# Optimization experiments

Measured on AMD Instinct MI355X. Metric: run time of the kernel, lower is better.

## Reference

```python
import jax, jax.numpy as jnp
import numpy as np

M, N, K, C, H = 100000, 8192, 32, 256, 8
DH = C // H
FF = 512
R = (15, 15, 7)  # 2*MAXRANGE-1 per axis for MAXRANGE=[8,8,4]


def _layer_norm(x, g, b, eps=1e-5):
    mu = jnp.mean(x, axis=-1, keepdims=True)
    xc = x - mu
    var = jnp.mean(xc * xc, axis=-1, keepdims=True)
    return xc * jax.lax.rsqrt(var + eps) * g + b


def setup_inputs() -> dict:
    key = jax.random.key(0)
    ks = iter(jax.random.split(key, 40))
    d = {}
    d['voxel_features'] = jax.random.normal(next(ks), (M, C), jnp.float32)
    d['query_coords'] = jax.random.normal(next(ks), (N, 3), jnp.float32)
    d['query_indices'] = jax.random.randint(next(ks), (N,), 0, M)
    d['gather_indices'] = jax.random.randint(next(ks), (N, K), 0, M)
    d['gather_mask'] = jax.random.randint(next(ks), (N, K), 0, 2).astype(bool)
    d['rel_x'] = jax.random.randint(next(ks), (N, K), 0, R[0])
    d['rel_y'] = jax.random.randint(next(ks), (N, K), 0, R[1])
    d['rel_z'] = jax.random.randint(next(ks), (N, K), 0, R[2])
    s = 0.02
    # pos_proj: Conv1d(3, C, 1) == linear on coords
    d['w_pos'] = jax.random.normal(next(ks), (3, C), jnp.float32) * s
    d['b_pos'] = jnp.zeros((C,), jnp.float32)
    for nm in ['q', 'k', 'v', 'proj']:
        d['w_' + nm] = jax.random.normal(next(ks), (C, C), jnp.float32) * (C ** -0.5)
        d['b_' + nm] = jnp.zeros((C,), jnp.float32)
    d['ln1_g'] = jnp.ones((C,), jnp.float32); d['ln1_b'] = jnp.zeros((C,), jnp.float32)
    d['ln2_g'] = jnp.ones((C,), jnp.float32); d['ln2_b'] = jnp.zeros((C,), jnp.float32)
    d['w_ff1'] = jax.random.normal(next(ks), (C, FF), jnp.float32) * (C ** -0.5)
    d['b_ff1'] = jnp.zeros((FF,), jnp.float32)
    d['w_ff2'] = jax.random.normal(next(ks), (FF, C), jnp.float32) * (FF ** -0.5)
    d['b_ff2'] = jnp.zeros((C,), jnp.float32)
    # per-axis relative position tables: [H, DH, 2W-1] for q-side and k-side
    for m in ['q', 'k']:
        for ax, r in zip(['x', 'y', 'z'], R):
            d[f'pos_{m}{ax}'] = jax.random.normal(next(ks), (H, DH, r), jnp.float32) * s
    return d


def reference(voxel_features, query_coords, query_indices, gather_indices, gather_mask,
              rel_x, rel_y, rel_z,
              w_pos, b_pos, w_q, b_q, w_k, b_k, w_v, b_v, w_proj, b_proj,
              ln1_g, ln1_b, ln2_g, ln2_b, w_ff1, b_ff1, w_ff2, b_ff2,
              pos_qx, pos_qy, pos_qz, pos_kx, pos_ky, pos_kz):
    x = _layer_norm(voxel_features, ln1_g, ln1_b)           # [M, C] pre-norm
    # gather window centers (queries) + positional projection of coords
    q_in = x[query_indices] + jax.nn.relu(query_coords @ w_pos + b_pos)  # [N, C]
    kv_in = x[gather_indices]                                # [N, K, C]
    kv_in = jnp.where(gather_mask[..., None], 0.0, kv_in)
    q = (q_in @ w_q + b_q).reshape(N, H, DH)
    k = (kv_in @ w_k + b_k).reshape(N, K, H, DH)
    v = (kv_in @ w_v + b_v).reshape(N, K, H, DH)
    logits = jnp.einsum('nhd,nkhd->nhk', q, k) * (DH ** -0.5)  # [N, H, K]
    # query-side per-axis relative position bias: contract q with table, gather at rel idx
    for pos, rel in ((pos_qx, rel_x), (pos_qy, rel_y), (pos_qz, rel_z)):
        qp = jnp.einsum('nhd,hdr->nhr', q, pos)              # [N, H, R]
        logits = logits + jnp.take_along_axis(qp, rel[:, None, :], axis=2)
    # key-side per-axis relative position bias
    for pos, rel in ((pos_kx, rel_x), (pos_ky, rel_y), (pos_kz, rel_z)):
        kp = jnp.einsum('nkhd,hdr->nkhr', k, pos)            # [N, K, H, R]
        bias = jnp.take_along_axis(kp, rel[:, :, None, None], axis=3)[..., 0]  # [N, K, H]
        logits = logits + bias.transpose(0, 2, 1)
    logits = jnp.where(gather_mask[:, None, :], -1e9, logits)
    attn = jax.nn.softmax(logits, axis=-1)
    out = jnp.einsum('nhk,nkhd->nhd', attn, v).reshape(N, C) @ w_proj + b_proj
    act = voxel_features[query_indices] + out                # residual (pre-norm block)
    h = jax.nn.relu(_layer_norm(act, ln2_g, ln2_b) @ w_ff1 + b_ff1) @ w_ff2 + b_ff2
    return act + h                                           # [N, C]
```

## Files before the change

### kernel.cpp

```cpp
#include <hip/hip_runtime.h>
#include <hip/hip_bf16.h>
#include <math.h>

#define MV   100000
#define NQ   8192
#define KN   32
#define CH   256
#define NH   8
#define DHD  32
#define FFD  512
#define NG   (NQ*KN)
#define QPW  37
#define QPN  (NH*QPW)
#define QPL  320
#define ASTR 40
#define KSTR 264

typedef __bf16 bf16x8 __attribute__((ext_vector_type(8)));
typedef float  f32x4  __attribute__((ext_vector_type(4)));

__device__ __forceinline__ float bf2f(unsigned short u) {
    return __uint_as_float(((unsigned int)u) << 16);
}
__device__ __forceinline__ unsigned short f2bf(float f) {
    unsigned int x = __float_as_uint(f);
    unsigned int r = x + 0x7FFFu + ((x >> 16) & 1u);
    return (unsigned short)(r >> 16);
}
__device__ __forceinline__ void glds16(const unsigned short* g, unsigned short* l) {
    __builtin_amdgcn_global_load_lds(
        (const __attribute__((address_space(1))) void*)g,
        (__attribute__((address_space(3))) void*)l, 16, 0, 0);
}

__global__ __launch_bounds__(256) void k_detect_mask(const unsigned char* __restrict__ raw,
                                                     int* __restrict__ flags) {
    __shared__ int any;
    if (threadIdx.x == 0) any = 0;
    __syncthreads();
    const uint4* p = (const uint4*)raw;
    int i = blockIdx.x * 256 + threadIdx.x;
    uint4 v = p[i];
    if ((v.x | v.y | v.z | v.w) & 0xFFFFFF00u) any = 1;
    __syncthreads();
    if (threadIdx.x == 0) flags[blockIdx.x] = any;
}

__global__ __launch_bounds__(256) void k_prep(const float* __restrict__ w_k,
                                              const float* __restrict__ w_v,
                                              const float* __restrict__ w_ff1,
                                              const float* __restrict__ w_ff2,
                                              const float* __restrict__ w_proj,
                                              const float* __restrict__ w_q,
                                              const float* __restrict__ b_k,
                                              const float* __restrict__ b_v,
                                              const float* __restrict__ pos_qx,
                                              const float* __restrict__ pos_qy,
                                              const float* __restrict__ pos_qz,
                                              const void* __restrict__ mask_raw,
                                              const int* __restrict__ gidx,
                                              const int* __restrict__ flags,
                                              unsigned short* __restrict__ w_kv_t,
                                              unsigned short* __restrict__ w1_t,
                                              unsigned short* __restrict__ w2_t,
                                              unsigned short* __restrict__ wp_t,
                                              unsigned short* __restrict__ wq_t,
                                              unsigned short* __restrict__ wqp_t,
                                              float* __restrict__ bkv,
                                              float* __restrict__ zbias,
                                              int* __restrict__ mask_i,
                                              unsigned char* __restrict__ touched) {
    __shared__ int bl;
    if (threadIdx.x == 0) {
        int a = 0;
        #pragma unroll 8
        for (int i = 0; i < 64; i++) a |= flags[i];
        bl = a;
    }
    __syncthreads();
    int byteLayout = bl;
    int idx = blockIdx.x * 256 + threadIdx.x;
    if (blockIdx.x == 0 && threadIdx.x < 512)
        bkv[threadIdx.x] = (threadIdx.x < 256) ? b_k[threadIdx.x]
                                               : b_v[threadIdx.x - 256];
    if (idx < QPL) zbias[idx] = 0.f;
    if (idx < NG) {
        int mv = byteLayout ? (int)((const unsigned char*)mask_raw)[idx]
                            : ((const int*)mask_raw)[idx];
        mask_i[idx] = (mv != 0) ? 1 : 0;
        if (mv == 0) touched[gidx[idx]] = 1;
    }
    if (idx < 512 * 256) {
        int col = idx >> 8, j = idx & 255;
        float v = (col < 256) ? w_k[j * 256 + col] : w_v[j * 256 + (col - 256)];
        w_kv_t[idx] = f2bf(v);
    }
    if (idx < 512 * 256) {
        int n = idx >> 8, k = idx & 255;
        w1_t[idx] = f2bf(w_ff1[k * FFD + n]);
    }
    if (idx < 256 * 512) {
        int n = idx >> 9, k = idx & 511;
        w2_t[idx] = f2bf(w_ff2[k * CH + n]);
    }
    if (idx < 256 * 256) {
        int n = idx >> 8, k = idx & 255;
        wp_t[idx] = f2bf(w_proj[k * CH + n]);
        wq_t[idx] = f2bf(w_q[k * CH + n]);
    }
    if (idx < QPL * 256) {
        int col = idx >> 8, k = idx & 255;
        float v = 0.f;
        if (col < QPN) {
            int h = col / QPW, r = col % QPW;
            int h2 = k >> 5, d = k & 31;
            if (h2 == h) {
                if (r < 15)      v = pos_qx[(h * DHD + d) * 15 + r];
                else if (r < 30) v = pos_qy[(h * DHD + d) * 15 + (r - 15)];
                else             v = pos_qz[(h * DHD + d) * 7  + (r - 30)];
            }
        }
        wqp_t[idx] = f2bf(v);
    }
}

__global__ __launch_bounds__(256) void k_posc(const float* __restrict__ pos_kx,
                                              const float* __restrict__ pos_ky,
                                              const float* __restrict__ pos_kz,
                                              float* __restrict__ comb) {
    int idx = blockIdx.x * 256 + threadIdx.x;
    if (idx >= 8 * 15 * 15 * 7 * 32) return;
    int d = idx & 31, r = idx >> 5;
    int rz = r % 7;  r /= 7;
    int ry = r % 15; r /= 15;
    int rx = r % 15; int h = r / 15;
    comb[idx] = pos_kx[(h * DHD + d) * 15 + rx]
              + pos_ky[(h * DHD + d) * 15 + ry]
              + pos_kz[(h * DHD + d) * 7  + rz];
}

__global__ __launch_bounds__(256) void k_ln(const float* __restrict__ x,
                                            const float* __restrict__ g,
                                            const float* __restrict__ b,
                                            unsigned short* __restrict__ o,
                                            int nrows) {
    int wid = threadIdx.x >> 6, lane = threadIdx.x & 63;
    int row = blockIdx.x * 4 + wid;
    if (row >= nrows) return;
    const float4 v = *(const float4*)(x + (size_t)row * CH + lane * 4);
    float s  = v.x + v.y + v.z + v.w;
    float sq = v.x * v.x + v.y * v.y + v.z * v.z + v.w * v.w;
    #pragma unroll
    for (int off = 1; off < 64; off <<= 1) {
        s  += __shfl_xor(s,  off);
        sq += __shfl_xor(sq, off);
    }
    float mu  = s * (1.f / CH);
    float var = sq * (1.f / CH) - mu * mu;
    float rs  = rsqrtf(var + 1e-5f);
    float4 gv = *(const float4*)(g + lane * 4);
    float4 bv = *(const float4*)(b + lane * 4);
    ushort4 ov;
    ov.x = f2bf((v.x - mu) * rs * gv.x + bv.x);
    ov.y = f2bf((v.y - mu) * rs * gv.y + bv.y);
    ov.z = f2bf((v.z - mu) * rs * gv.z + bv.z);
    ov.w = f2bf((v.w - mu) * rs * gv.w + bv.w);
    *(ushort4*)(o + (size_t)row * CH + lane * 4) = ov;
}

__global__ __launch_bounds__(256) void k_qin(const unsigned short* __restrict__ ln_x,
                                             const float* __restrict__ coords,
                                             const int* __restrict__ qidx,
                                             const float* __restrict__ w_pos,
                                             const float* __restrict__ b_pos,
                                             unsigned short* __restrict__ qin) {
    int c = threadIdx.x;
    int nb = blockIdx.x * 8;
    float wp0 = w_pos[c], wp1 = w_pos[CH + c], wp2 = w_pos[2 * CH + c], bp = b_pos[c];
    #pragma unroll
    for (int qq = 0; qq < 8; qq++) {
        int n = nb + qq;
        float p = bp + coords[n * 3] * wp0 + coords[n * 3 + 1] * wp1 + coords[n * 3 + 2] * wp2;
        p = fmaxf(p, 0.f);
        int qi = qidx[n];
        qin[(size_t)n * CH + c] = f2bf(bf2f(ln_x[(size_t)qi * CH + c]) + p);
    }
}

__global__ __launch_bounds__(256) void k_kv(const unsigned short* __restrict__ ln_x,
                                            const unsigned short* __restrict__ w_kv_t,
                                            const float* __restrict__ bkv,
                                            const unsigned char* __restrict__ touched,
                                            unsigned short* __restrict__ kv) {
    __shared__ __align__(16) unsigned short As[8 * 4096];
    __shared__ __align__(16) unsigned short Bs[4096];
    const int tid = threadIdx.x;
    const int w = tid >> 6, l = tid & 63;
    const int wr = w >> 1, wc = w & 1;
    const int rowbase = blockIdx.x * 128;
    const int sr = l >> 2, sq = l & 3;
    const int ml = l & 15, qd = l >> 4;

    int ra0 = rowbase + w * 16 + sr;
    int ra1 = rowbase + 64 + w * 16 + sr;
    int ok0 = (ra0 < MV) && touched[ra0 < MV ? ra0 : 0];
    int ok1 = (ra1 < MV) && touched[ra1 < MV ? ra1 : 0];
    const unsigned short* pa0 = ln_x + (size_t)(ok0 ? ra0 : rowbase) * CH + sq * 8;
    const unsigned short* pa1 = ln_x + (size_t)(ok1 ? ra1 : rowbase) * CH + sq * 8;
    unsigned short* lA0 = As + w * 512;
    unsigned short* lA1 = As + 2048 + w * 512;
    unsigned short* lB0 = Bs + w * 512;
    unsigned short* lB1 = Bs + 2048 + w * 512;

    #pragma unroll
    for (int c = 0; c < 8; c++) {
        glds16(pa0 + c * 32, lA0 + c * 4096);
        glds16(pa1 + c * 32, lA1 + c * 4096);
    }

    for (int ct = 0; ct < 4; ct++) {
        const int col0 = ct * 128;
        const unsigned short* pb0 = w_kv_t + (size_t)(col0 + w * 16 + sr) * CH + sq * 8;
        const unsigned short* pb1 = w_kv_t + (size_t)(col0 + 64 + w * 16 + sr) * CH + sq * 8;
        f32x4 acc[4][4];
        #pragma unroll
        for (int mt = 0; mt < 4; mt++)
            #pragma unroll
            for (int nt = 0; nt < 4; nt++)
                acc[mt][nt] = (f32x4){0.f, 0.f, 0.f, 0.f};

        for (int c = 0; c < 8; c++) {
            __syncthreads();
            glds16(pb0 + c * 32, lB0);
            glds16(pb1 + c * 32, lB1);
            __syncthreads();
            bf16x8 af[4], bf[4];
            const unsigned short* Ac = As + c * 4096;
            #pragma unroll
            for (int mt = 0; mt < 4; mt++)
                af[mt] = *(const bf16x8*)(Ac + (wr * 64 + mt * 16 + ml) * 32 + qd * 8);
            #pragma unroll
            for (int nt = 0; nt < 4; nt++)
                bf[nt] = *(const bf16x8*)(Bs + (wc * 64 + nt * 16 + ml) * 32 + qd * 8);
            #pragma unroll
            for (int mt = 0; mt < 4; mt++)
                #pragma unroll
                for (int nt = 0; nt < 4; nt++)
                    acc[mt][nt] = __builtin_amdgcn_mfma_f32_16x16x32_bf16(af[mt], bf[nt], acc[mt][nt], 0, 0, 0);
        }

        float bb[4];
        #pragma unroll
        for (int nt = 0; nt < 4; nt++)
            bb[nt] = bkv[col0 + wc * 64 + nt * 16 + ml];
        #pragma unroll
        for (int mt = 0; mt < 4; mt++) {
            __syncthreads();
            #pragma unroll
            for (int nt = 0; nt < 4; nt++) {
                int lcol = wc * 64 + nt * 16 + ml;
                #pragma unroll
                for (int i = 0; i < 4; i++)
                    Bs[wr * 2048 + (qd * 4 + i) * 128 + lcol] = f2bf(acc[mt][nt][i] + bb[nt]);
            }
            __syncthreads();
            int rl = tid >> 4, cc = (tid & 15) * 8;
            int g0 = rowbase + mt * 16 + rl;
            int g1 = rowbase + 64 + mt * 16 + rl;
            if (g0 < MV && touched[g0])
                *(uint4*)(kv + (size_t)g0 * 512 + col0 + cc) = *(const uint4*)(Bs + rl * 128 + cc);
            if (g1 < MV && touched[g1])
                *(uint4*)(kv + (size_t)g1 * 512 + col0 + cc) = *(const uint4*)(Bs + 2048 + rl * 128 + cc);
        }
    }
}

template <int KD, int EPI, int LDO>
__global__ __launch_bounds__(256) void k_mm(const unsigned short* __restrict__ A,
                                            const unsigned short* __restrict__ Bt_g,
                                            const float* __restrict__ bias,
                                            const float* __restrict__ res,
                                            const int* __restrict__ qidx,
                                            unsigned short* __restrict__ out_bf,
                                            float* __restrict__ out_f) {
    __shared__ __align__(16) unsigned short As[128 * ASTR];
    __shared__ __align__(16) unsigned short Bs[64 * ASTR];
    int tid = threadIdx.x;
    int w = tid >> 6, l = tid & 63;
    int rowbase = blockIdx.y * 128;
    int col0 = blockIdx.x * 64;
    int r0 = tid >> 2, qt = tid & 3;
    const unsigned short* a0p = A + (size_t)(rowbase + r0) * KD + qt * 8;
    const unsigned short* a1p = A + (size_t)(rowbase + 64 + r0) * KD + qt * 8;

    f32x4 acc[2][4];
    #pragma unroll
    for (int mt = 0; mt < 2; mt++)
        #pragma unroll
        for (int nt = 0; nt < 4; nt++)
            acc[mt][nt] = (f32x4){0.f, 0.f, 0.f, 0.f};

    const int ml = l & 15, qd = l >> 4;
    for (int kk = 0; kk < KD; kk += 32) {
        __syncthreads();
        uint4 v0 = *(const uint4*)(a0p + kk);
        uint4 v1 = *(const uint4*)(a1p + kk);
        *(uint4*)(As + r0 * ASTR + qt * 8)        = v0;
        *(uint4*)(As + (64 + r0) * ASTR + qt * 8) = v1;
        {
            uint4 bv = *(const uint4*)(Bt_g + (size_t)(col0 + r0) * KD + kk + qt * 8);
            *(uint4*)(Bs + r0 * ASTR + qt * 8) = bv;
        }
        __syncthreads();
        bf16x8 a0 = *(const bf16x8*)(As + (w * 32 + ml) * ASTR + qd * 8);
        bf16x8 a1 = *(const bf16x8*)(As + (w * 32 + 16 + ml) * ASTR + qd * 8);
        #pragma unroll
        for (int nt = 0; nt < 4; nt++) {
            bf16x8 bb = *(const bf16x8*)(Bs + (nt * 16 + ml) * ASTR + qd * 8);
            acc[0][nt] = __builtin_amdgcn_mfma_f32_16x16x32_bf16(a0, bb, acc[0][nt], 0, 0, 0);
            acc[1][nt] = __builtin_amdgcn_mfma_f32_16x16x32_bf16(a1, bb, acc[1][nt], 0, 0, 0);
        }
    }

    #pragma unroll
    for (int nt = 0; nt < 4; nt++) {
        int col = col0 + nt * 16 + ml;
        float bv = bias[col];
        #pragma unroll
        for (int mt = 0; mt < 2; mt++) {
            int rl = w * 32 + mt * 16 + qd * 4;
            #pragma unroll
            for (int i = 0; i < 4; i++) {
                int row = rowbase + rl + i;
                float v = acc[mt][nt][i] + bv;
                if (EPI == 0) {
                    out_bf[(size_t)row * LDO + col] = f2bf(fmaxf(v, 0.f));
                } else if (EPI == 1) {
                    out_f[(size_t)row * CH + col] = v + res[(size_t)row * CH + col];
                } else if (EPI == 2) {
                    int qi = qidx[row];
                    out_f[(size_t)row * CH + col] = v + res[(size_t)qi * CH + col];
                } else if (EPI == 3) {
                    out_f[(size_t)row * CH + col] = v;
                    out_bf[(size_t)row * CH + col] = f2bf(v);
                } else {
                    out_f[(size_t)row * LDO + col] = v;
                }
            }
        }
    }
}

__global__ __launch_bounds__(256) void k_attn3(const float* __restrict__ qbuf,
                                               const float* __restrict__ qp,
                                               const unsigned short* __restrict__ kvmat,
                                               const int* __restrict__ gidx,
                                               const int* __restrict__ mask_i,
                                               const int* __restrict__ rel_x,
                                               const int* __restrict__ rel_y,
                                               const int* __restrict__ rel_z,
                                               const float* __restrict__ comb,
                                               const float* __restrict__ b_v,
                                               unsigned short* __restrict__ attnln) {
    __shared__ float q_s[2 * 256];
    __shared__ float qp_s[2 * QPL];
    __shared__ float attn_s[2 * 256];
    __shared__ int   mask_s[64];
    __shared__ int   gidx_s[64];
    __shared__ __align__(16) unsigned short ks[64 * KSTR];

    int tid = threadIdx.x;
    int qb = blockIdx.x * 2;
    for (int i = tid; i < 512; i += 256) q_s[i] = qbuf[(size_t)qb * CH + i];
    for (int i = tid; i < 2 * QPL; i += 256) qp_s[i] = qp[(size_t)qb * QPL + i];
    if (tid < 64) {
        mask_s[tid] = mask_i[qb * 32 + tid];
        gidx_s[tid] = gidx[qb * 32 + tid];
    }
    __syncthreads();

    const int srow = tid >> 5;
    const int schk = tid & 31;
    uint4 kreg[8];
    #pragma unroll
    for (int j = 0; j < 8; j++) {
        int r = j * 8 + srow;
        uint4 v = {0u, 0u, 0u, 0u};
        if (!mask_s[r])
            v = *(const uint4*)(kvmat + (size_t)gidx_s[r] * 512 + schk * 8);
        kreg[j] = v;
    }
    #pragma unroll
    for (int j = 0; j < 8; j++)
        *(uint4*)(ks + (j * 8 + srow) * KSTR + schk * 8) = kreg[j];
    __syncthreads();

    int h = tid >> 5, k = tid & 31;
    const float scale = 0.17677669529663687f;
    for (int qq = 0; qq < 2; qq++) {
        int n = qb + qq;
        int gi = n * KN + k;
        int r = qq * 32 + k;
        int mk = mask_s[r];
        float lg = -1e9f;
        if (!mk) {
            int rx = rel_x[gi], ry = rel_y[gi], rz = rel_z[gi];
            const unsigned short* kp = ks + r * KSTR + h * 32;
            float kv[32];
            #pragma unroll
            for (int j = 0; j < 4; j++) {
                uint4 u = *(const uint4*)(kp + j * 8);
                kv[j * 8 + 0] = bf2f((unsigned short)(u.x & 0xFFFF));
                kv[j * 8 + 1] = bf2f((unsigned short)(u.x >> 16));
                kv[j * 8 + 2] = bf2f((unsigned short)(u.y & 0xFFFF));
                kv[j * 8 + 3] = bf2f((unsigned short)(u.y >> 16));
                kv[j * 8 + 4] = bf2f((unsigned short)(u.z & 0xFFFF));
                kv[j * 8 + 5] = bf2f((unsigned short)(u.z >> 16));
                kv[j * 8 + 6] = bf2f((unsigned short)(u.w & 0xFFFF));
                kv[j * 8 + 7] = bf2f((unsigned short)(u.w >> 16));
            }
            const float* cp = comb + ((((h * 15 + rx) * 15 + ry) * 7 + rz) << 5);
            float s1 = 0.f, s2 = 0.f;
            const float* qrow = q_s + qq * CH + h * DHD;
            #pragma unroll
            for (int d = 0; d < 32; d++) {
                s1 += kv[d] * qrow[d];
                s2 += kv[d] * cp[d];
            }
            lg = s1 * scale + s2
               + qp_s[qq * QPL + h * QPW + rx]
               + qp_s[qq * QPL + h * QPW + 15 + ry]
               + qp_s[qq * QPL + h * QPW + 30 + rz];
        }
        float mx = lg;
        #pragma unroll
        for (int off = 1; off <= 16; off <<= 1) mx = fmaxf(mx, __shfl_xor(mx, off));
        float e = mk ? 0.f : __expf(lg - mx);
        float sm = e;
        #pragma unroll
        for (int off = 1; off <= 16; off <<= 1) sm += __shfl_xor(sm, off);
        attn_s[qq * 256 + tid] = (sm > 0.f) ? e / sm : 0.f;
    }

    #pragma unroll
    for (int j = 0; j < 8; j++) {
        int r = j * 8 + srow;
        uint4 v = {0u, 0u, 0u, 0u};
        if (!mask_s[r])
            v = *(const uint4*)(kvmat + (size_t)gidx_s[r] * 512 + 256 + schk * 8);
        kreg[j] = v;
    }
    __syncthreads();
    #pragma unroll
    for (int j = 0; j < 8; j++)
        *(uint4*)(ks + (j * 8 + srow) * KSTR + schk * 8) = kreg[j];
    __syncthreads();

    int w = tid >> 6, l = tid & 63;
    int q2 = w >> 1, kh = w & 1;
    int hh = l >> 3;
    float a0 = 0.f, a1 = 0.f, a2 = 0.f, a3 = 0.f;
    #pragma unroll
    for (int i = 0; i < 16; i++) {
        int kk = kh * 16 + i;
        int r = q2 * 32 + kk;
        float av = attn_s[q2 * 256 + hh * 32 + kk];
        ushort4 v4 = *(const ushort4*)(ks + r * KSTR + l * 4);
        a0 += av * bf2f(v4.x);
        a1 += av * bf2f(v4.y);
        a2 += av * bf2f(v4.z);
        a3 += av * bf2f(v4.w);
    }
    if (kh == 1) {
        float4 pv = {a0, a1, a2, a3};
        *(float4*)(qp_s + q2 * 256 + l * 4) = pv;
    }
    __syncthreads();
    if (kh == 0) {
        float4 pv = *(const float4*)(qp_s + q2 * 256 + l * 4);
        a0 += pv.x; a1 += pv.y; a2 += pv.z; a3 += pv.w;
        int nm = 0;
        #pragma unroll
        for (int kk = 0; kk < 32; kk++) nm += 1 - mask_s[q2 * 32 + kk];
        int col = l * 4;
        if (nm == 0) {
            a0 = b_v[col]; a1 = b_v[col + 1]; a2 = b_v[col + 2]; a3 = b_v[col + 3];
        }
        ushort4 o;
        o.x = f2bf(a0); o.y = f2bf(a1); o.z = f2bf(a2); o.w = f2bf(a3);
        *(ushort4*)(attnln + (size_t)(qb + q2) * CH + col) = o;
    }
}

extern "C" void kernel_launch(void* const* d_in, const int* in_sizes, int n_in,
                              void* d_out, int out_size, void* d_ws, size_t ws_size,
                              hipStream_t stream) {
    (void)in_sizes; (void)n_in; (void)out_size; (void)ws_size;
    const float* vox    = (const float*)d_in[0];
    const float* coords = (const float*)d_in[1];
    const int*   qidx   = (const int*)d_in[2];
    const int*   gidx   = (const int*)d_in[3];
    const void*  mraw   = d_in[4];
    const int*   rel_x  = (const int*)d_in[5];
    const int*   rel_y  = (const int*)d_in[6];
    const int*   rel_z  = (const int*)d_in[7];
    const float* w_pos  = (const float*)d_in[8];
    const float* b_pos  = (const float*)d_in[9];
    const float* w_q    = (const float*)d_in[10];
    const float* b_q    = (const float*)d_in[11];
    const float* w_k    = (const float*)d_in[12];
    const float* b_k    = (const float*)d_in[13];
    const float* w_v    = (const float*)d_in[14];
    const float* b_v    = (const float*)d_in[15];
    const float* w_proj = (const float*)d_in[16];
    const float* b_proj = (const float*)d_in[17];
    const float* ln1_g  = (const float*)d_in[18];
    const float* ln1_b  = (const float*)d_in[19];
    const float* ln2_g  = (const float*)d_in[20];
    const float* ln2_b  = (const float*)d_in[21];
    const float* w_ff1  = (const float*)d_in[22];
    const float* b_ff1  = (const float*)d_in[23];
    const float* w_ff2  = (const float*)d_in[24];
    const float* b_ff2  = (const float*)d_in[25];
    const float* pos_qx = (const float*)d_in[26];
    const float* pos_qy = (const float*)d_in[27];
    const float* pos_qz = (const float*)d_in[28];
    const float* pos_kx = (const float*)d_in[29];
    const float* pos_ky = (const float*)d_in[30];
    const float* pos_kz = (const float*)d_in[31];

    char* p = (char*)d_ws;
    auto take = [&](size_t n) { char* r = p; p += (n + 255) & ~(size_t)255; return r; };
    unsigned short* ln_x    = (unsigned short*)take((size_t)MV * CH * 2);
    unsigned short* w_kv_t  = (unsigned short*)take((size_t)512 * 256 * 2);
    unsigned short* w1_t    = (unsigned short*)take((size_t)512 * 256 * 2);
    unsigned short* w2_t    = (unsigned short*)take((size_t)256 * 512 * 2);
    unsigned short* wp_t    = (unsigned short*)take((size_t)256 * 256 * 2);
    unsigned short* wq_t    = (unsigned short*)take((size_t)256 * 256 * 2);
    unsigned short* wqp_t   = (unsigned short*)take((size_t)QPL * 256 * 2);
    float*          bkv     = (float*)take(512 * 4);
    float*          zbias   = (float*)take(QPL * 4);
    int*            flags   = (int*)take(64 * 4);
    int*            mask_i  = (int*)take((size_t)NG * 4);
    unsigned char*  touched = (unsigned char*)take(MV);
    float*          comb    = (float*)take((size_t)8 * 15 * 15 * 7 * 32 * 4);
    unsigned short* qin     = (unsigned short*)take((size_t)NQ * CH * 2);
    float*          qbuf    = (float*)take((size_t)NQ * CH * 4);
    unsigned short* qbf     = (unsigned short*)take((size_t)NQ * CH * 2);
    float*          qp      = (float*)take((size_t)NQ * QPL * 4);
    unsigned short* kvmat   = (unsigned short*)take((size_t)MV * 512 * 2);
    unsigned short* attnln  = (unsigned short*)take((size_t)NQ * CH * 2);
    float*          actbuf  = (float*)take((size_t)NQ * CH * 4);
    unsigned short* actln   = (unsigned short*)take((size_t)NQ * CH * 2);
    unsigned short* hbuf    = (unsigned short*)take((size_t)NQ * FFD * 2);

    hipMemsetAsync(touched, 0, MV, stream);
    hipLaunchKernelGGL(k_detect_mask, dim3(64), dim3(256), 0, stream,
                       (const unsigned char*)mraw, flags);
    hipLaunchKernelGGL(k_prep, dim3(NG / 256), dim3(256), 0, stream,
                       w_k, w_v, w_ff1, w_ff2, w_proj, w_q, b_k, b_v,
                       pos_qx, pos_qy, pos_qz, mraw, gidx, flags,
                       w_kv_t, w1_t, w2_t, wp_t, wq_t, wqp_t, bkv, zbias,
                       mask_i, touched);
    hipLaunchKernelGGL(k_posc, dim3((8 * 15 * 15 * 7 * 32 + 255) / 256), dim3(256), 0, stream,
                       pos_kx, pos_ky, pos_kz, comb);
    hipLaunchKernelGGL(k_ln, dim3(MV / 4 + 1), dim3(256), 0, stream,
                       vox, ln1_g, ln1_b, ln_x, MV);
    hipLaunchKernelGGL(k_qin, dim3(NQ / 8), dim3(256), 0, stream,
                       ln_x, coords, qidx, w_pos, b_pos, qin);
    hipLaunchKernelGGL(k_kv, dim3((MV + 127) / 128), dim3(256), 0, stream,
                       ln_x, w_kv_t, bkv, touched, kvmat);
    hipLaunchKernelGGL(HIP_KERNEL_NAME(k_mm<256, 3, CH>), dim3(4, NQ / 128), dim3(256), 0, stream,
                       qin, wq_t, b_q, (const float*)nullptr, (const int*)nullptr,
                       qbf, qbuf);
    hipLaunchKernelGGL(HIP_KERNEL_NAME(k_mm<256, 4, QPL>), dim3(QPL / 64, NQ / 128), dim3(256), 0, stream,
                       qbf, wqp_t, zbias, (const float*)nullptr, (const int*)nullptr,
                       (unsigned short*)nullptr, qp);
    hipLaunchKernelGGL(k_attn3, dim3(NQ / 2), dim3(256), 0, stream,
                       qbuf, qp, kvmat, gidx, mask_i, rel_x, rel_y, rel_z,
                       comb, b_v, attnln);
    hipLaunchKernelGGL(HIP_KERNEL_NAME(k_mm<256, 2, CH>), dim3(4, NQ / 128), dim3(256), 0, stream,
                       attnln, wp_t, b_proj, vox, qidx,
                       (unsigned short*)nullptr, actbuf);
    hipLaunchKernelGGL(k_ln, dim3(NQ / 4), dim3(256), 0, stream,
                       actbuf, ln2_g, ln2_b, actln, NQ);
    hipLaunchKernelGGL(HIP_KERNEL_NAME(k_mm<256, 0, FFD>), dim3(8, NQ / 128), dim3(256), 0, stream,
                       actln, w1_t, b_ff1, (const float*)nullptr, (const int*)nullptr,
                       hbuf, (float*)nullptr);
    hipLaunchKernelGGL(HIP_KERNEL_NAME(k_mm<512, 1, CH>), dim3(4, NQ / 128), dim3(256), 0, stream,
                       hbuf, w2_t, b_ff2, actbuf, (const int*)nullptr,
                       (unsigned short*)nullptr, (float*)d_out);
}
```

Baseline: 401.8 us.

## Skip LayerNorm on unreferenced voxels and split KV GEMM columns across blocks

Marks query-index rows as touched in the prep kernel, so the first LayerNorm can skip voxel rows that no gather or query ever reads. This saves fp32 reads and bf16 writes on those rows. The KV projection kernel now uses a 2D grid with one 128-column tile per block instead of looping over four column tiles. Its shared memory drops from about 72KB to 16KB, which should allow more resident blocks, at the cost of reloading the A rows four times.

```diff
diff --git a/kernel.cpp b/kernel.cpp
--- a/kernel.cpp
+++ b/kernel.cpp
@@ -59,6 +59,7 @@
                                               const float* __restrict__ pos_qz,
                                               const void* __restrict__ mask_raw,
                                               const int* __restrict__ gidx,
+                                              const int* __restrict__ qidx,
                                               const int* __restrict__ flags,
                                               unsigned short* __restrict__ w_kv_t,
                                               unsigned short* __restrict__ w1_t,
@@ -84,6 +85,7 @@
         bkv[threadIdx.x] = (threadIdx.x < 256) ? b_k[threadIdx.x]
                                                : b_v[threadIdx.x - 256];
     if (idx < QPL) zbias[idx] = 0.f;
+    if (idx < NQ) touched[qidx[idx]] = 1;
     if (idx < NG) {
         int mv = byteLayout ? (int)((const unsigned char*)mask_raw)[idx]
                             : ((const int*)mask_raw)[idx];
@@ -142,11 +144,13 @@
 __global__ __launch_bounds__(256) void k_ln(const float* __restrict__ x,
                                             const float* __restrict__ g,
                                             const float* __restrict__ b,
+                                            const unsigned char* __restrict__ tch,
                                             unsigned short* __restrict__ o,
                                             int nrows) {
     int wid = threadIdx.x >> 6, lane = threadIdx.x & 63;
     int row = blockIdx.x * 4 + wid;
     if (row >= nrows) return;
+    if (tch && !tch[row]) return;
     const float4 v = *(const float4*)(x + (size_t)row * CH + lane * 4);
     float s  = v.x + v.y + v.z + v.w;
     float sq = v.x * v.x + v.y * v.y + v.z * v.z + v.w * v.w;
@@ -192,86 +196,79 @@
                                             const float* __restrict__ bkv,
                                             const unsigned char* __restrict__ touched,
                                             unsigned short* __restrict__ kv) {
-    __shared__ __align__(16) unsigned short As[8 * 4096];
-    __shared__ __align__(16) unsigned short Bs[4096];
+    __shared__ __align__(16) unsigned short As[128 * 32];
+    __shared__ __align__(16) unsigned short Bs[128 * 32];
     const int tid = threadIdx.x;
     const int w = tid >> 6, l = tid & 63;
     const int wr = w >> 1, wc = w & 1;
-    const int rowbase = blockIdx.x * 128;
+    const int rowbase = blockIdx.y * 128;
+    const int col0 = blockIdx.x * 128;
     const int sr = l >> 2, sq = l & 3;
-    const int ml = l & 15, qd = l >> 4;
-
     int ra0 = rowbase + w * 16 + sr;
     int ra1 = rowbase + 64 + w * 16 + sr;
     int ok0 = (ra0 < MV) && touched[ra0 < MV ? ra0 : 0];
     int ok1 = (ra1 < MV) && touched[ra1 < MV ? ra1 : 0];
-    const unsigned short* pa0 = ln_x + (size_t)(ok0 ? ra0 : rowbase) * CH + sq * 8;
-    const unsigned short* pa1 = ln_x + (size_t)(ok1 ? ra1 : rowbase) * CH + sq * 8;
+    const unsigned short* pa0 = ln_x + (size_t)(ok0 ? ra0 : 0) * CH + sq * 8;
+    const unsigned short* pa1 = ln_x + (size_t)(ok1 ? ra1 : 0) * CH + sq * 8;
+    const unsigned short* pb0 = w_kv_t + (size_t)(col0 + w * 16 + sr) * CH + sq * 8;
+    const unsigned short* pb1 = w_kv_t + (size_t)(col0 + 64 + w * 16 + sr) * CH + sq * 8;
     unsigned short* lA0 = As + w * 512;
     unsigned short* lA1 = As + 2048 + w * 512;
     unsigned short* lB0 = Bs + w * 512;
     unsigned short* lB1 = Bs + 2048 + w * 512;
 
-    #pragma unroll
-    for (int c = 0; c < 8; c++) {
-        glds16(pa0 + c * 32, lA0 + c * 4096);
-        glds16(pa1 + c * 32, lA1 + c * 4096);
-    }
-
-    for (int ct = 0; ct < 4; ct++) {
-        const int col0 = ct * 128;
-        const unsigned short* pb0 = w_kv_t + (size_t)(col0 + w * 16 + sr) * CH + sq * 8;
-        const unsigned short* pb1 = w_kv_t + (size_t)(col0 + 64 + w * 16 + sr) * CH + sq * 8;
-        f32x4 acc[4][4];
+    f32x4 acc[4][4];
+    #pragma unroll
+    for (int mt = 0; mt < 4; mt++)
+        #pragma unroll
+        for (int nt = 0; nt < 4; nt++)
+            acc[mt][nt] = (f32x4){0.f, 0.f, 0.f, 0.f};
+
+    const int ml = l & 15, qd = l >> 4;
+    for (int kk = 0; kk < CH; kk += 32) {
+        __syncthreads();
+        glds16(pa0 + kk, lA0);
+        glds16(pa1 + kk, lA1);
+        glds16(pb0 + kk, lB0);
+        glds16(pb1 + kk, lB1);
+        __syncthreads();
+        bf16x8 af[4], bf[4];
+        #pragma unroll
+        for (int mt = 0; mt < 4; mt++)
+            af[mt] = *(const bf16x8*)(As + (wr * 64 + mt * 16 + ml) * 32 + qd * 8);
+        #pragma unroll
+        for (int nt = 0; nt < 4; nt++)
+            bf[nt] = *(const bf16x8*)(Bs + (wc * 64 + nt * 16 + ml) * 32 + qd * 8);
         #pragma unroll
         for (int mt = 0; mt < 4; mt++)
             #pragma unroll
             for (int nt = 0; nt < 4; nt++)
-                acc[mt][nt] = (f32x4){0.f, 0.f, 0.f, 0.f};
-
-        for (int c = 0; c < 8; c++) {
-            __syncthreads();
-            glds16(pb0 + c * 32, lB0);
-            glds16(pb1 + c * 32, lB1);
-            __syncthreads();
-            bf16x8 af[4], bf[4];
-            const unsigned short* Ac = As + c * 4096;
+                acc[mt][nt] = __builtin_amdgcn_mfma_f32_16x16x32_bf16(af[mt], bf[nt], acc[mt][nt], 0, 0, 0);
+    }
+
+    float bb[4];
+    #pragma unroll
+    for (int nt = 0; nt < 4; nt++)
+        bb[nt] = bkv[col0 + wc * 64 + nt * 16 + ml];
+    unsigned short* trs = As;
+    #pragma unroll
+    for (int mt = 0; mt < 4; mt++) {
+        __syncthreads();
+        #pragma unroll
+        for (int nt = 0; nt < 4; nt++) {
+            int lcol = wc * 64 + nt * 16 + ml;
             #pragma unroll
-            for (int mt = 0; mt < 4; mt++)
-                af[mt] = *(const bf16x8*)(Ac + (wr * 64 + mt * 16 + ml) * 32 + qd * 8);
-            #pragma unroll
-            for (int nt = 0; nt < 4; nt++)
-                bf[nt] = *(const bf16x8*)(Bs + (wc * 64 + nt * 16 + ml) * 32 + qd * 8);
-            #pragma unroll
-            for (int mt = 0; mt < 4; mt++)
-                #pragma unroll
-                for (int nt = 0; nt < 4; nt++)
-                    acc[mt][nt] = __builtin_amdgcn_mfma_f32_16x16x32_bf16(af[mt], bf[nt], acc[mt][nt], 0, 0, 0);
-        }
-
-        float bb[4];
-        #pragma unroll
-        for (int nt = 0; nt < 4; nt++)
-            bb[nt] = bkv[col0 + wc * 64 + nt * 16 + ml];
-        #pragma unroll
-        for (int mt = 0; mt < 4; mt++) {
-            __syncthreads();
-            #pragma unroll
-            for (int nt = 0; nt < 4; nt++) {
-                int lcol = wc * 64 + nt * 16 + ml;
-                #pragma unroll
-                for (int i = 0; i < 4; i++)
-                    Bs[wr * 2048 + (qd * 4 + i) * 128 + lcol] = f2bf(acc[mt][nt][i] + bb[nt]);
-            }
-            __syncthreads();
-            int rl = tid >> 4, cc = (tid & 15) * 8;
-            int g0 = rowbase + mt * 16 + rl;
-            int g1 = rowbase + 64 + mt * 16 + rl;
-            if (g0 < MV && touched[g0])
-                *(uint4*)(kv + (size_t)g0 * 512 + col0 + cc) = *(const uint4*)(Bs + rl * 128 + cc);
-            if (g1 < MV && touched[g1])
-                *(uint4*)(kv + (size_t)g1 * 512 + col0 + cc) = *(const uint4*)(Bs + 2048 + rl * 128 + cc);
-        }
+            for (int i = 0; i < 4; i++)
+                trs[wr * 2048 + (qd * 4 + i) * 128 + lcol] = f2bf(acc[mt][nt][i] + bb[nt]);
+        }
+        __syncthreads();
+        int rl = tid >> 4, cc = (tid & 15) * 8;
+        int g0 = rowbase + mt * 16 + rl;
+        int g1 = rowbase + 64 + mt * 16 + rl;
+        if (g0 < MV && touched[g0])
+            *(uint4*)(kv + (size_t)g0 * 512 + col0 + cc) = *(const uint4*)(trs + rl * 128 + cc);
+        if (g1 < MV && touched[g1])
+            *(uint4*)(kv + (size_t)g1 * 512 + col0 + cc) = *(const uint4*)(trs + 2048 + rl * 128 + cc);
     }
 }
 
@@ -559,16 +556,16 @@
                        (const unsigned char*)mraw, flags);
     hipLaunchKernelGGL(k_prep, dim3(NG / 256), dim3(256), 0, stream,
                        w_k, w_v, w_ff1, w_ff2, w_proj, w_q, b_k, b_v,
-                       pos_qx, pos_qy, pos_qz, mraw, gidx, flags,
+                       pos_qx, pos_qy, pos_qz, mraw, gidx, qidx, flags,
                        w_kv_t, w1_t, w2_t, wp_t, wq_t, wqp_t, bkv, zbias,
                        mask_i, touched);
     hipLaunchKernelGGL(k_posc, dim3((8 * 15 * 15 * 7 * 32 + 255) / 256), dim3(256), 0, stream,
                        pos_kx, pos_ky, pos_kz, comb);
     hipLaunchKernelGGL(k_ln, dim3(MV / 4 + 1), dim3(256), 0, stream,
-                       vox, ln1_g, ln1_b, ln_x, MV);
+                       vox, ln1_g, ln1_b, touched, ln_x, MV);
     hipLaunchKernelGGL(k_qin, dim3(NQ / 8), dim3(256), 0, stream,
                        ln_x, coords, qidx, w_pos, b_pos, qin);
-    hipLaunchKernelGGL(k_kv, dim3((MV + 127) / 128), dim3(256), 0, stream,
+    hipLaunchKernelGGL(k_kv, dim3(4, (MV + 127) / 128), dim3(256), 0, stream,
                        ln_x, w_kv_t, bkv, touched, kvmat);
     hipLaunchKernelGGL(HIP_KERNEL_NAME(k_mm<256, 3, CH>), dim3(4, NQ / 128), dim3(256), 0, stream,
                        qin, wq_t, b_q, (const float*)nullptr, (const int*)nullptr,
@@ -583,7 +580,7 @@
                        attnln, wp_t, b_proj, vox, qidx,
                        (unsigned short*)nullptr, actbuf);
     hipLaunchKernelGGL(k_ln, dim3(NQ / 4), dim3(256), 0, stream,
-                       actbuf, ln2_g, ln2_b, actln, NQ);
+                       actbuf, ln2_g, ln2_b, (const unsigned char*)nullptr, actln, NQ);
     hipLaunchKernelGGL(HIP_KERNEL_NAME(k_mm<256, 0, FFD>), dim3(8, NQ / 128), dim3(256), 0, stream,
                        actln, w1_t, b_ff1, (const float*)nullptr, (const int*)nullptr,
                        hbuf, (float*)nullptr);
```

New measurement: 391.1 us. 1.03x faster.
